# Optimization experiments

Measured on AMD Instinct MI355X. Metric: run time of the kernel, lower is better.

Reference implementation:

```python
import jax, jax.numpy as jnp
import numpy as np

B = 4096
T = 50          # relaxation steps
EPS = 0.5       # epsilon_ep
SCALE = 1.0     # output_scale
CH = [32, 64, 64, 256]


def _conv(x, w, b, stride):
    # NCHW conv, k=3, pad=1 (matches nn.Conv2d(k=3, stride, padding=1))
    y = jax.lax.conv_general_dilated(
        x, w, (stride, stride), [(1, 1), (1, 1)],
        dimension_numbers=("NCHW", "OIHW", "NCHW"))
    return y + b[None, :, None, None]


def _energy(x, s1, s2, s3, s4, vb, w1, b1, w2, b2, w3, b3, w4, b4):
    # E = 0.5*sum||s^n||^2 (incl. x) - Phi_coupling, per sample -> (B,)
    # activation = identity, spectral_scale = 1.0
    n = x.shape[0]
    sq = lambda t: 0.5 * jnp.sum(t.reshape(n, -1) ** 2, axis=1)
    quad = sq(x) + sq(s1) + sq(s2) + sq(s3) + sq(s4)
    dot = lambda a, c: jnp.sum((a * c).reshape(n, -1), axis=1)
    phi = dot(vb, x)                              # visible bias term
    phi = phi + dot(s1, _conv(x, w1, b1, 2))      # s1 . w1(s0)
    phi = phi + dot(s2, _conv(s1, w2, b2, 2))     # s2 . w2(s1)
    phi = phi + dot(s3, _conv(s2, w3, b3, 1))     # s3 . w3(s2)
    phi = phi + jnp.sum(s4 * (s3.reshape(n, -1) @ w4.T + b4), axis=1)
    return quad - phi


def setup_inputs() -> dict:
    key = jax.random.key(0)
    ks = jax.random.split(key, 6)
    x = jax.random.normal(ks[0], (B, 1, 28, 28), jnp.float32)
    # scaled-down Xavier-ish init so the identity-activation relaxation contracts
    def w(k, shape, fan_in):
        return jax.random.normal(k, shape, jnp.float32) * np.float32(0.5 / np.sqrt(fan_in))
    w1 = w(ks[1], (CH[0], 1, 3, 3), 1 * 9)
    w2 = w(ks[2], (CH[1], CH[0], 3, 3), CH[0] * 9)
    w3 = w(ks[3], (CH[2], CH[1], 3, 3), CH[1] * 9)
    w4 = w(ks[4], (CH[3], CH[2] * 7 * 7), CH[2] * 49)
    vb = jax.random.normal(ks[5], (1, 1, 28, 28), jnp.float32) * 0.01
    return dict(x=x, vb=vb,
                w1=w1, b1=jnp.zeros((CH[0],), jnp.float32),
                w2=w2, b2=jnp.zeros((CH[1],), jnp.float32),
                w3=w3, b3=jnp.zeros((CH[2],), jnp.float32),
                w4=w4, b4=jnp.zeros((CH[3],), jnp.float32))


def reference(x, vb, w1, b1, w2, b2, w3, b3, w4, b4):
    n = x.shape[0]
    s0 = (jnp.zeros((n, CH[0], 14, 14), jnp.float32),
          jnp.zeros((n, CH[1], 7, 7), jnp.float32),
          jnp.zeros((n, CH[2], 7, 7), jnp.float32),
          jnp.zeros((n, CH[3]), jnp.float32))

    def e_sum(s):
        return jnp.sum(_energy(x, s[0], s[1], s[2], s[3],
                               vb, w1, b1, w2, b2, w3, b3, w4, b4))

    def step(s, _):
        g = jax.grad(e_sum)(s)
        return tuple(si - EPS * gi for si, gi in zip(s, g)), None

    s_star, _ = jax.lax.scan(step, s0, None, length=T)
    out = _energy(x, s_star[0], s_star[1], s_star[2], s_star[3],
                  vb, w1, b1, w2, b2, w3, b3, w4, b4) * SCALE
    return out  # (B,)
```

## Files before the change

kernel.cpp:

```cpp
#include <hip/hip_runtime.h>
#include <cstddef>


typedef unsigned short ushort_t;
typedef __attribute__((ext_vector_type(8))) short bf8_t;
typedef __attribute__((ext_vector_type(4))) float f4_t;

#define MFMA16 __builtin_amdgcn_mfma_f32_16x16x32_bf16

#define NBn 832
#define NITER 50
#define GPL 5218304u

#define SELG 13125632u
#define R1G 399360
#define R2G 6043648
#define R3G 9877504
#define R4G 12912640

#define W2F_OFF 0u
#define W2B_OFF 36864u
#define W3F_OFF 73728u
#define W3B_OFF 147456u
#define W4P_OFF 221184u
#define W4Q_OFF 1826816u
#define W2PL 18432u
#define W3PL 36864u
#define W4PL 802816u
#define ZOFF 3432448u
#define WPTOT2 3435008u

__device__ __forceinline__ void bsplit(float v, ushort_t& h, ushort_t& lo) {
  union { float f; unsigned u; } a; a.f = v;
  unsigned uh = (a.u + 0x7fffu + ((a.u >> 16) & 1u)) & 0xffff0000u;
  h = (ushort_t)(uh >> 16);
  union { unsigned u; float f; } b; b.u = uh;
  float r = v - b.f;
  union { float f; unsigned u; } c; c.f = r;
  lo = (ushort_t)((c.u + 0x7fffu + ((c.u >> 16) & 1u)) >> 16);
}

__device__ __forceinline__ ushort_t bround(float v) {
  union { float f; unsigned u; } a; a.f = v;
  return (ushort_t)((a.u + 0x7fffu + ((a.u >> 16) & 1u)) >> 16);
}

__device__ __forceinline__ float b2f(ushort_t h) {
  union { unsigned u; float f; } a; a.u = ((unsigned)h) << 16;
  return a.f;
}

__device__ __forceinline__ float bjoin(ushort_t h, ushort_t l) {
  return b2f(h) + b2f(l);
}

__device__ __forceinline__ int xswz(int lin, int nwg) {
  int xcd = lin & 7, o = lin >> 3;
  int q = nwg >> 3, r = nwg & 7;
  return (xcd < r) ? (xcd * (q + 1) + o) : (r * (q + 1) + (xcd - r) * q + o);
}

__global__ void k_fill0(float* p, unsigned n) {
  for (unsigned i = blockIdx.x * blockDim.x + threadIdx.x; i < n;
       i += gridDim.x * blockDim.x)
    p[i] = 0.f;
}

__global__ void k_pack2(const float* __restrict__ w2, ushort_t* __restrict__ WP) {
  int idx = blockIdx.x * blockDim.x + threadIdx.x;
  if (idx >= 18432) return;
  int co = idx / 288, rem = idx % 288, ci = rem / 9, t = rem % 9;
  ushort_t h, l; bsplit(w2[idx], h, l);
  unsigned f = W2F_OFF + t * 2048 + co * 32 + ci;
  unsigned b = W2B_OFF + t * 2048 + ci * 64 + co;
  WP[f] = h; WP[f + W2PL] = l;
  WP[b] = h; WP[b + W2PL] = l;
}

__global__ void k_pack3(const float* __restrict__ w3, ushort_t* __restrict__ WP) {
  int idx = blockIdx.x * blockDim.x + threadIdx.x;
  if (idx >= 36864) return;
  int co = idx / 576, rem = idx % 576, ci = rem / 9, t = rem % 9;
  ushort_t h, l; bsplit(w3[idx], h, l);
  unsigned f = W3F_OFF + t * 4096 + co * 64 + ci;
  unsigned b = W3B_OFF + t * 4096 + ci * 64 + co;
  WP[f] = h; WP[f + W3PL] = l;
  WP[b] = h; WP[b + W3PL] = l;
}

__global__ void k_pack4(const float* __restrict__ w4, ushort_t* __restrict__ WP) {
  int idx = blockIdx.x * blockDim.x + threadIdx.x;
  if (idx >= 802816) return;
  int o = idx / 3136, kk = idx % 3136, c = kk / 49, p = kk % 49;
  ushort_t h, l; bsplit(w4[idx], h, l);
  unsigned a = W4P_OFF + p * 16384 + c * 256 + o;
  unsigned b = W4Q_OFF + o * 3136 + p * 64 + c;
  WP[a] = h; WP[a + W4PL] = l;
  WP[b] = h; WP[b + W4PL] = l;
}

__global__ void k_u1b(ushort_t* __restrict__ G, const float* __restrict__ w1,
                      const float* __restrict__ b1) {
  unsigned idx = blockIdx.x * blockDim.x + threadIdx.x;
  if (idx >= GPL) return;
  int q = idx / 26624, rem = idx % 26624, n = rem / 32, c = rem % 32;
  int oy = q / 14, ox = q % 14;
  float v = 0.f;
  if (n < 784) {
    int py = n / 28, px = n % 28;
    int ky = py - (2 * oy - 1), kx = px - (2 * ox - 1);
    if (ky >= 0 && ky < 3 && kx >= 0 && kx < 3) v = w1[c * 9 + ky * 3 + kx];
  } else if (n == 784) {
    v = b1[c];
  }
  ushort_t h, l; bsplit(v, h, l);
  G[idx] = h; G[idx + GPL] = l;
}

__global__ void k_p1(ushort_t* __restrict__ D, const ushort_t* __restrict__ S,
                     const ushort_t* __restrict__ G) {
  unsigned g8 = (blockIdx.x * blockDim.x + threadIdx.x) * 8;
  if (g8 >= GPL) return;
  size_t off = (size_t)R1G + g8;
  bf8_t oh = *(const bf8_t*)&S[off];
  bf8_t gh = *(const bf8_t*)&G[g8], gl = *(const bf8_t*)&G[g8 + GPL];
  bf8_t rh, rl;
#pragma unroll
  for (int e = 0; e < 8; ++e) {
    float v = 0.5f * b2f((ushort_t)oh[e]) -
              bjoin((ushort_t)gh[e], (ushort_t)gl[e]);
    ushort_t h, l; bsplit(v, h, l);
    rh[e] = (short)h; rl[e] = (short)l;
  }
  *(bf8_t*)&D[off] = rh;
  *(bf8_t*)&D[off + SELG] = rl;
}

struct Ent { unsigned eh, el; int b; int ars, brs; };

__device__ __forceinline__ Ent entry(int role, int e, int p, int mt, int post) {
  Ent E;
  if (role == 3) {
    E.eh = W4Q_OFF + ((unsigned)mt * 64u) * 3136u + (unsigned)e * 32u;
    E.el = E.eh + W4PL;
    E.b = R3G + (e >> 1) * 53248 + (e & 1) * 32;
    E.ars = 3136; E.brs = 64;
  } else if (role == 2) {
    int y = p / 7, x = p % 7;
    if (e < 18) {
      int t = e >> 1, sub = e & 1, ky = t / 3, kx = t % 3;
      int iy = y - 1 + ky, ix = x - 1 + kx;
      bool v = (iy >= 0 && iy < 7 && ix >= 0 && ix < 7);
      E.eh = v ? (W3F_OFF + t * 4096u + sub * 32u) : ZOFF;
      E.el = v ? (E.eh + W3PL) : ZOFF;
      E.b = R2G + (iy * 7 + ix) * 53248 + sub * 32;
      E.ars = v ? 64 : 32; E.brs = 64;
    } else {
      int s = e - 18;
      E.eh = W4P_OFF + (unsigned)p * 16384u + s * 32u;
      E.el = E.eh + W4PL;
      E.b = R4G + s * 32;
      E.ars = 256; E.brs = 256;
    }
  } else if (role == 1) {
    int y = p / 7, x = p % 7;
    if (e < 9) {
      int ky = e / 3, kx = e % 3;
      int iy = 2 * y - 1 + ky, ix = 2 * x - 1 + kx;
      bool v = (iy >= 0 && iy < 14 && ix >= 0 && ix < 14);
      E.eh = v ? (W2F_OFF + e * 2048u) : ZOFF;
      E.el = v ? (E.eh + W2PL) : ZOFF;
      E.b = R1G + (iy * 14 + ix) * 26624;
      E.ars = 32; E.brs = 32;
    } else if (e < 27 && !post) {
      int u = e - 9, t = u >> 1, sub = u & 1, ky = t / 3, kx = t % 3;
      int ty = y + 1 - ky, tx = x + 1 - kx;
      bool v = (ty >= 0 && ty < 7 && tx >= 0 && tx < 7);
      E.eh = v ? (W3B_OFF + t * 4096u + sub * 32u) : ZOFF;
      E.el = v ? (E.eh + W3PL) : ZOFF;
      E.b = R3G + (ty * 7 + tx) * 53248 + sub * 32;
      E.ars = v ? 64 : 32; E.brs = 64;
    } else {
      E.eh = ZOFF; E.el = ZOFF; E.b = R4G; E.ars = 32; E.brs = 256;
    }
  } else {
    int y = p / 14, x = p % 14;
    int tj = e >> 1, sub = e & 1, jy = tj >> 1, jx = tj & 1;
    int ky = (y & 1) ? 2 * jy : 1;
    int kx = (x & 1) ? 2 * jx : 1;
    bool py_ = (y & 1) || (jy == 0);
    bool px_ = (x & 1) || (jx == 0);
    int oy = (y + 1 - ky) >> 1, ox = (x + 1 - kx) >> 1;
    bool v = py_ && px_ && oy >= 0 && oy < 7 && ox >= 0 && ox < 7;
    int t = ky * 3 + kx;
    E.eh = v ? (W2B_OFF + t * 2048u + sub * 32u) : ZOFF;
    E.el = v ? (E.eh + W2PL) : ZOFF;
    E.b = R2G + (oy * 7 + ox) * 53248 + sub * 32;
    E.ars = v ? 64 : 32; E.brs = 64;
  }
  return E;
}

__device__ __forceinline__ Ent entryg(int role, int e, int p, int mt, int post,
                                      int elim) {
  if (e >= elim) {
    Ent E; E.eh = ZOFF; E.el = ZOFF; E.b = R4G; E.ars = 32; E.brs = 256;
    return E;
  }
  return entry(role, e, p, mt, post);
}

template <int APL, int MI>
__device__ __forceinline__ void loadA(bf8_t (&A0)[MI][APL], bf8_t (&A1)[MI][APL],
                                      int role, int e0, int p, int mt, int post,
                                      int elim, int mhalf, int lm, int koff,
                                      const ushort_t* __restrict__ WP) {
  Ent E0 = entryg(role, e0, p, mt, post, elim);
  Ent E1 = entryg(role, e0 + 1, p, mt, post, elim);
#pragma unroll
  for (int mi = 0; mi < MI; ++mi) {
    int mo0 = (mhalf + mi * 16 + lm) * E0.ars + koff;
    int mo1 = (mhalf + mi * 16 + lm) * E1.ars + koff;
    A0[mi][0] = *(const bf8_t*)(WP + E0.eh + mo0);
    A1[mi][0] = *(const bf8_t*)(WP + E1.eh + mo1);
    if (APL == 2) {
      A0[mi][APL - 1] = *(const bf8_t*)(WP + E0.el + mo0);
      A1[mi][APL - 1] = *(const bf8_t*)(WP + E1.el + mo1);
    }
  }
}

__device__ __forceinline__ void loadB(bf8_t& s0, bf8_t& s1, int role, int e0,
                                      int p, int mt, int post, int elim, int n0,
                                      int sn, int sc,
                                      const ushort_t* __restrict__ S) {
  Ent E0 = entryg(role, e0, p, mt, post, elim);
  Ent E1 = entryg(role, e0 + 1, p, mt, post, elim);
  s0 = *(const bf8_t*)(S + E0.b + (n0 + sn) * E0.brs + sc);
  s1 = *(const bf8_t*)(S + E1.b + (n0 + sn) * E1.brs + sc);
}

template <int APL, int MI, int NJ>
__device__ __forceinline__ void mfmaset(const bf8_t (&A0)[MI][APL],
                                        const bf8_t (&A1)[MI][APL],
                                        const ushort_t* __restrict__ Bb, int nhalf,
                                        int lm, int koff, f4_t (&acc)[MI][NJ]) {
#pragma unroll
  for (int nj = 0; nj < NJ; ++nj) {
    int lo = (nhalf + nj * 16 + lm) * 40 + koff;
    bf8_t b0 = *(const bf8_t*)&Bb[lo];
    bf8_t b1 = *(const bf8_t*)&Bb[2560 + lo];
#pragma unroll
    for (int mi = 0; mi < MI; ++mi)
#pragma unroll
      for (int pl = 0; pl < APL; ++pl) {
        acc[mi][nj] = MFMA16(A0[mi][pl], b0, acc[mi][nj], 0, 0, 0);
        acc[mi][nj] = MFMA16(A1[mi][pl], b1, acc[mi][nj], 0, 0, 0);
      }
  }
}

template <int APL, int MI, int NJ>
__device__ __forceinline__ void mloop(int role, int post, int p, int mt, int n0,
                                      int NC2, int mhalf, int nhalf,
                                      const ushort_t* __restrict__ S,
                                      const ushort_t* __restrict__ WP,
                                      ushort_t* __restrict__ SB,
                                      f4_t (&acc)[MI][NJ]) {
  const int tid = threadIdx.x, l = tid & 63;
  const int lm = l & 15, koff = (l >> 4) * 8;
  const int sn = tid >> 2, sc = (tid & 3) * 8;
  const int elim = 2 * NC2;
  bf8_t bs0[4], bs1[4];
#pragma unroll
  for (int q = 0; q < 4; ++q)
    loadB(bs0[q], bs1[q], role, 2 * q, p, mt, post, elim, n0, sn, sc, S);
  bf8_t aE0[MI][APL], aE1[MI][APL], aO0[MI][APL], aO1[MI][APL];
  loadA<APL, MI>(aE0, aE1, role, 0, p, mt, post, elim, mhalf, lm, koff, WP);
  loadA<APL, MI>(aO0, aO1, role, 2, p, mt, post, elim, mhalf, lm, koff, WP);
  {
    int wb = sn * 40 + sc;
    *(bf8_t*)&SB[wb] = bs0[0];
    *(bf8_t*)&SB[wb + 2560] = bs1[0];
  }
  __syncthreads();
  const int ntrip = (NC2 + 3) >> 2;
  for (int t4 = 0; t4 < ntrip; ++t4) {
    int j4 = t4 * 4;
#pragma unroll
    for (int pp = 0; pp < 4; ++pp) {
      int jj = j4 + pp;
      loadB(bs0[pp], bs1[pp], role, 2 * (jj + 4), p, mt, post, elim, n0, sn, sc, S);
      const ushort_t* Bb = SB + (pp & 1) * 5120;
      if ((pp & 1) == 0) {
        mfmaset<APL, MI, NJ>(aE0, aE1, Bb, nhalf, lm, koff, acc);
        loadA<APL, MI>(aE0, aE1, role, 2 * (jj + 2), p, mt, post, elim, mhalf, lm,
                       koff, WP);
      } else {
        mfmaset<APL, MI, NJ>(aO0, aO1, Bb, nhalf, lm, koff, acc);
        loadA<APL, MI>(aO0, aO1, role, 2 * (jj + 2), p, mt, post, elim, mhalf, lm,
                       koff, WP);
      }
      {
        int wb = sn * 40 + sc;
        ushort_t* Wb = SB + ((pp + 1) & 1) * 5120;
        *(bf8_t*)&Wb[wb] = bs0[(pp + 1) & 3];
        *(bf8_t*)&Wb[wb + 2560] = bs1[(pp + 1) & 3];
      }
      __syncthreads();
    }
  }
}

template <int POST>
__global__ __launch_bounds__(256) void k_mega(
    const ushort_t* __restrict__ S, ushort_t* __restrict__ D,
    const ushort_t* __restrict__ G, const ushort_t* __restrict__ WP,
    const float* __restrict__ b2, const float* __restrict__ b3,
    const float* __restrict__ b4) {
  __shared__ __align__(16) ushort_t SB[10240];
  float* Lt = (float*)SB;
  const int tid = threadIdx.x, l = tid & 63, w = tid >> 6;
  const int lm = l & 15, lk = l >> 4;
  int b = blockIdx.x;
  int role, rb, ntile, pq;
  if (b < 52) { role = 3; rb = xswz(b, 52); ntile = rb >> 2; pq = rb & 3; }
  else if (b < 689) { role = 2; rb = xswz(b - 52, 637); ntile = rb / 49; pq = rb % 49; }
  else if (b < 1326) { role = 1; rb = xswz(b - 689, 637); ntile = rb / 49; pq = rb % 49; }
  else { role = 0; rb = xswz(b - 1326, 2548); ntile = rb / 196; pq = rb % 196; }

  int n0 = ntile * 64;

  if (role == 0) {
    f4_t acc[2][1] = {};
    mloop<1, 2, 1>(0, POST, pq, 0, n0, 4, 0, w * 16, S, WP, SB, acc);
    __syncthreads();
#pragma unroll
    for (int mi = 0; mi < 2; ++mi)
#pragma unroll
      for (int r = 0; r < 4; ++r)
        Lt[(w * 16 + lm) * 33 + mi * 16 + lk * 4 + r] = acc[mi][0][r];
    __syncthreads();
    int nl = tid >> 2, cq = (tid & 3) * 8;
    int n = n0 + nl;
    size_t off = (size_t)R1G + (size_t)pq * 26624 + (size_t)n * 32 + cq;
    size_t goff = (size_t)pq * 26624 + (size_t)n * 32 + cq;
    bf8_t oh = *(const bf8_t*)&S[off];
    bf8_t gh = *(const bf8_t*)&G[goff], gl = *(const bf8_t*)&G[goff + GPL];
    const float* lp = Lt + nl * 33 + cq;
    bf8_t rh;
#pragma unroll
    for (int e = 0; e < 8; ++e) {
      float old = b2f((ushort_t)oh[e]);
      float u = bjoin((ushort_t)gh[e], (ushort_t)gl[e]);
      rh[e] = (short)bround(0.5f * old + 0.5f * (lp[e] + u));
    }
    *(bf8_t*)&D[off] = rh;
  } else {
    f4_t acc[2][2] = {};
    int NC2 = (role == 3) ? 49 : (role == 2) ? (POST ? 9 : 13) : (POST ? 5 : 14);
    mloop<POST + 1, 2, 2>(role, POST, pq, pq, n0, NC2, (w & 1) * 32, (w >> 1) * 32,
                          S, WP, SB, acc);
    __syncthreads();
#pragma unroll
    for (int mi = 0; mi < 2; ++mi)
#pragma unroll
      for (int nj = 0; nj < 2; ++nj)
#pragma unroll
        for (int r = 0; r < 4; ++r)
          Lt[((w >> 1) * 32 + nj * 16 + lm) * 65 + (w & 1) * 32 + mi * 16 + lk * 4 + r] =
              acc[mi][nj][r];
    __syncthreads();
    int nl = tid >> 2, cq = (tid & 3) * 16;
    int n = n0 + nl;
    size_t off;
    const float* bias;
    int bq = cq;
    if (role == 1) { off = (size_t)R2G + (size_t)pq * 53248 + (size_t)n * 64 + cq; bias = b2; }
    else if (role == 2) { off = (size_t)R3G + (size_t)pq * 53248 + (size_t)n * 64 + cq; bias = b3; }
    else { off = (size_t)R4G + (size_t)n * 256 + pq * 64 + cq; bias = b4; bq = pq * 64 + cq; }
    const float* lp = Lt + nl * 65 + cq;
#pragma unroll
    for (int half = 0; half < 2; ++half) {
      size_t o8 = off + half * 8;
      bf8_t oh = *(const bf8_t*)&S[o8];
      bf8_t rh, rl;
#pragma unroll
      for (int e = 0; e < 8; ++e) {
        float v = lp[half * 8 + e];
        if (n == 784) v += bias[bq + half * 8 + e];
        float old = b2f((ushort_t)oh[e]);
        if (POST) {
          float nv = 0.5f * old - v;
          ushort_t h, l2; bsplit(nv, h, l2);
          rh[e] = (short)h; rl[e] = (short)l2;
        } else {
          rh[e] = (short)bround(0.5f * old + 0.5f * v);
        }
      }
      *(bf8_t*)&D[o8] = rh;
      if (POST) *(bf8_t*)&D[o8 + SELG] = rl;
    }
  }
}

__device__ __forceinline__ void hstep(int s, size_t& base, int& C, int& c0) {
  if (s < 196) { base = R1G + (size_t)s * 26624; C = 32; c0 = 0; }
  else if (s < 294) { int u = s - 196; base = R2G + (size_t)(u >> 1) * 53248; C = 64; c0 = (u & 1) * 32; }
  else if (s < 392) { int u = s - 294; base = R3G + (size_t)(u >> 1) * 53248; C = 64; c0 = (u & 1) * 32; }
  else { base = R4G; C = 256; c0 = (s - 392) * 32; }
}

struct HF { bf8_t ah[4]; bf8_t al[4]; bf8_t b[4]; };

__device__ __forceinline__ void hload(HF& F, int s, int m0, int n0, int lm, int koff,
                                      const ushort_t* __restrict__ P,
                                      const ushort_t* __restrict__ S) {
  size_t base; int C, c0;
  hstep(s, base, C, c0);
#pragma unroll
  for (int mi = 0; mi < 4; ++mi) {
    const ushort_t* Am = P + base + (size_t)(m0 + mi * 16 + lm) * C + c0 + koff;
    F.ah[mi] = *(const bf8_t*)Am;
    F.al[mi] = *(const bf8_t*)(Am + SELG);
  }
#pragma unroll
  for (int nj = 0; nj < 4; ++nj)
    F.b[nj] = *(const bf8_t*)(S + base + (size_t)(n0 + nj * 16 + lm) * C + c0 + koff);
}

__device__ __forceinline__ void hmfma(HF& F, f4_t (&acc)[4][4]) {
#pragma unroll
  for (int mi = 0; mi < 4; ++mi)
#pragma unroll
    for (int nj = 0; nj < 4; ++nj) {
      acc[mi][nj] = MFMA16(F.ah[mi], F.b[nj], acc[mi][nj], 0, 0, 0);
      acc[mi][nj] = MFMA16(F.al[mi], F.b[nj], acc[mi][nj], 0, 0, 0);
    }
}

__global__ __launch_bounds__(256) void k_hgemm(float* __restrict__ HpT,
                                               const ushort_t* __restrict__ P,
                                               const ushort_t* __restrict__ S) {
  int tid = threadIdx.x, l = tid & 63, w = tid >> 6;
  int lm = l & 15, lk = l >> 4, koff = lk * 8;
  int m0 = blockIdx.y * 128 + (w & 1) * 64;
  int n0 = blockIdx.x * 128 + (w >> 1) * 64;
  int z = blockIdx.z;
  int s0 = (400 * z) / 9, s1e = (400 * (z + 1)) / 9;
  int ns = s1e - s0;
  f4_t acc[4][4] = {};
  HF F0, F1;
  hload(F0, s0, m0, n0, lm, koff, P, S);
  hload(F1, (ns > 1) ? s0 + 1 : s0, m0, n0, lm, koff, P, S);
  int t = 0;
  for (; t + 2 <= ns; t += 2) {
    hmfma(F0, acc);
    hload(F0, (s0 + t + 2 < s1e) ? s0 + t + 2 : s1e - 1, m0, n0, lm, koff, P, S);
    hmfma(F1, acc);
    hload(F1, (s0 + t + 3 < s1e) ? s0 + t + 3 : s1e - 1, m0, n0, lm, koff, P, S);
  }
  if (t < ns) hmfma(F0, acc);
#pragma unroll
  for (int mi = 0; mi < 4; ++mi)
#pragma unroll
    for (int nj = 0; nj < 4; ++nj)
#pragma unroll
      for (int r = 0; r < 4; ++r) {
        int m = m0 + mi * 16 + lk * 4 + r;
        int n = n0 + nj * 16 + lm;
        if (m < NBn && n < NBn)
          HpT[((size_t)z * NBn + n) * NBn + m] = acc[mi][nj][r];
      }
}

__global__ void k_combT(ushort_t* __restrict__ HtH, ushort_t* __restrict__ HtL,
                        const float* __restrict__ HpT) {
  int idx = blockIdx.x * blockDim.x + threadIdx.x;
  if (idx >= NBn * NBn) return;
  float s = 0.f;
#pragma unroll
  for (int z = 0; z < 9; ++z) s += HpT[(size_t)z * NBn * NBn + idx];
  ushort_t h, l; bsplit(s, h, l);
  HtH[idx] = h; HtL[idx] = l;
}

__global__ void k_xsplit(ushort_t* __restrict__ XH, ushort_t* __restrict__ XL,
                         const float* __restrict__ x, int Bn) {
  int idx = blockIdx.x * blockDim.x + threadIdx.x;
  if (idx >= Bn * NBn) return;
  int i = idx / NBn, j = idx % NBn;
  float v = (j < 784) ? x[(size_t)i * 784 + j] : (j == 784 ? 1.f : 0.f);
  ushort_t h, l; bsplit(v, h, l);
  XH[idx] = h; XL[idx] = l;
}

__global__ __launch_bounds__(256) void k_ygemm(float* __restrict__ Y,
    const ushort_t* __restrict__ XH, const ushort_t* __restrict__ XL,
    const ushort_t* __restrict__ HtH, const ushort_t* __restrict__ HtL, int Bn) {
  int tid = threadIdx.x, l = tid & 63, w = tid >> 6;
  int lm = l & 15, lk = l >> 4, koff = lk * 8;
  int m0 = blockIdx.y * 64 + (w & 1) * 32;
  int n0 = blockIdx.x * 64 + (w >> 1) * 32;
  f4_t acc[2][2] = {};
  for (int k0 = 0; k0 < NBn; k0 += 32) {
    bf8_t bh[2], bl[2];
#pragma unroll
    for (int nj = 0; nj < 2; ++nj) {
      size_t bo = (size_t)(n0 + nj * 16 + lm) * NBn + k0 + koff;
      bh[nj] = *(const bf8_t*)(HtH + bo);
      bl[nj] = *(const bf8_t*)(HtL + bo);
    }
#pragma unroll
    for (int mi = 0; mi < 2; ++mi) {
      int mrow = m0 + mi * 16 + lm;
      if (mrow >= Bn) mrow = Bn - 1;
      size_t ao = (size_t)mrow * NBn + k0 + koff;
      bf8_t ah = *(const bf8_t*)(XH + ao);
      bf8_t al = *(const bf8_t*)(XL + ao);
#pragma unroll
      for (int nj = 0; nj < 2; ++nj) {
        acc[mi][nj] = MFMA16(ah, bh[nj], acc[mi][nj], 0, 0, 0);
        acc[mi][nj] = MFMA16(ah, bl[nj], acc[mi][nj], 0, 0, 0);
        acc[mi][nj] = MFMA16(al, bh[nj], acc[mi][nj], 0, 0, 0);
      }
    }
  }
#pragma unroll
  for (int mi = 0; mi < 2; ++mi)
#pragma unroll
    for (int nj = 0; nj < 2; ++nj)
#pragma unroll
      for (int r = 0; r < 4; ++r) {
        int m = m0 + mi * 16 + lk * 4 + r;
        int n = n0 + nj * 16 + lm;
        if (m < Bn) Y[(size_t)m * NBn + n] = acc[mi][nj][r];
      }
}

__global__ void k_out(float* __restrict__ out, const float* __restrict__ x,
                      const float* __restrict__ vb, const float* __restrict__ Y, int Bn) {
  int wave = threadIdx.x >> 6, lane = threadIdx.x & 63;
  int i = blockIdx.x * 4 + wave;
  if (i >= Bn) return;
  const float* xi = x + (size_t)i * 784;
  const float* yi = Y + (size_t)i * NBn;
  float s = 0.f;
  for (int j = lane; j < 784; j += 64) {
    float xv = xi[j];
    s += xv * (0.5f * xv - vb[j] + yi[j]);
  }
  for (int off = 32; off; off >>= 1) s += __shfl_down(s, off);
  if (lane == 0) out[i] = s + yi[784];
}

extern "C" void kernel_launch(void* const* d_in, const int* in_sizes, int n_in, void* d_out,
                              int out_size, void* d_ws, size_t ws_size, hipStream_t stream) {
  const float* x  = (const float*)d_in[0];
  const float* vb = (const float*)d_in[1];
  const float* w1 = (const float*)d_in[2];
  const float* b1 = (const float*)d_in[3];
  const float* w2 = (const float*)d_in[4];
  const float* b2 = (const float*)d_in[5];
  const float* w3 = (const float*)d_in[6];
  const float* b3 = (const float*)d_in[7];
  const float* w4 = (const float*)d_in[8];
  const float* b4 = (const float*)d_in[9];
  int Bn = in_sizes[0] / 784;
  float* out = (float*)d_out;

  ushort_t* S0 = (ushort_t*)d_ws;
  ushort_t* S1 = S0 + (size_t)SELG;
  ushort_t* Pb = S1 + (size_t)SELG;
  ushort_t* G  = Pb + (size_t)2 * SELG;
  ushort_t* WP = G + (size_t)2 * GPL;
  ushort_t* HtH = WP + WPTOT2;
  ushort_t* HtL = HtH + (size_t)NBn * NBn;
  float* HpT = (float*)S1;
  ushort_t* XH = Pb;
  ushort_t* XL = XH + (size_t)Bn * NBn;
  float* Y = (float*)G;

  const int TB = 256;
  k_fill0<<<2048, TB, 0, stream>>>((float*)S0, SELG / 2);
  k_fill0<<<2048, TB, 0, stream>>>((float*)S1, SELG / 2);
  k_fill0<<<2, TB, 0, stream>>>((float*)(WP + ZOFF), 1280);
  k_pack2<<<72, TB, 0, stream>>>(w2, WP);
  k_pack3<<<144, TB, 0, stream>>>(w3, WP);
  k_pack4<<<3136, TB, 0, stream>>>(w4, WP);
  k_u1b<<<20384, TB, 0, stream>>>(G, w1, b1);

  ushort_t* cur = S0;
  ushort_t* nxt = S1;
  for (int it = 0; it < NITER; ++it) {
    k_mega<0><<<3874, TB, 0, stream>>>(cur, nxt, G, WP, b2, b3, b4);
    ushort_t* t = cur; cur = nxt; nxt = t;
  }

  k_p1<<<2548, TB, 0, stream>>>(Pb, cur, G);
  k_mega<1><<<1326, TB, 0, stream>>>(cur, Pb, G, WP, b2, b3, b4);

  k_hgemm<<<dim3(7, 7, 9), TB, 0, stream>>>(HpT, Pb, cur);
  k_combT<<<(NBn * NBn + TB - 1) / TB, TB, 0, stream>>>(HtH, HtL, HpT);

  k_xsplit<<<(Bn * NBn + TB - 1) / TB, TB, 0, stream>>>(XH, XL, x, Bn);
  k_ygemm<<<dim3(13, (Bn + 63) / 64), TB, 0, stream>>>(Y, XH, XL, HtH, HtL, Bn);
  k_out<<<(Bn + 3) / 4, TB, 0, stream>>>(out, x, vb, Y, Bn);
}
```

Measured before the change: 3.609 ms.

## Process two K-steps per LDS stage to halve barriers in GEMM main loop

Restructures the software pipeline of the shared GEMM loop so each LDS buffer holds two K-slices and each barrier covers two MFMA sets instead of one. The LDS tile grows to double capacity and the global prefetch is reorganized into two ping-pong register sets. This aims to halve __syncthreads overhead per K, at the cost of more LDS per block, which may reduce occupancy. Odd slice counts may be handled less cleanly.

```diff
diff --git a/kernel.cpp b/kernel.cpp
--- a/kernel.cpp
+++ b/kernel.cpp
@@ -271,42 +271,61 @@
   const int lm = l & 15, koff = (l >> 4) * 8;
   const int sn = tid >> 2, sc = (tid & 3) * 8;
   const int elim = 2 * NC2;
-  bf8_t bs0[4], bs1[4];
-#pragma unroll
-  for (int q = 0; q < 4; ++q)
-    loadB(bs0[q], bs1[q], role, 2 * q, p, mt, post, elim, n0, sn, sc, S);
+  const int wb = sn * 40 + sc;
+  bf8_t pA0[2], pA1[2], pB0[2], pB1[2];
+#pragma unroll
+  for (int q = 0; q < 2; ++q)
+    loadB(pA0[q], pA1[q], role, 2 * q, p, mt, post, elim, n0, sn, sc, S);
+#pragma unroll
+  for (int q = 0; q < 2; ++q)
+    loadB(pB0[q], pB1[q], role, 4 + 2 * q, p, mt, post, elim, n0, sn, sc, S);
   bf8_t aE0[MI][APL], aE1[MI][APL], aO0[MI][APL], aO1[MI][APL];
   loadA<APL, MI>(aE0, aE1, role, 0, p, mt, post, elim, mhalf, lm, koff, WP);
   loadA<APL, MI>(aO0, aO1, role, 2, p, mt, post, elim, mhalf, lm, koff, WP);
   {
-    int wb = sn * 40 + sc;
-    *(bf8_t*)&SB[wb] = bs0[0];
-    *(bf8_t*)&SB[wb + 2560] = bs1[0];
-  }
+    *(bf8_t*)&SB[wb] = pA0[0];         *(bf8_t*)&SB[wb + 2560] = pA1[0];
+    *(bf8_t*)&SB[wb + 5120] = pA0[1];  *(bf8_t*)&SB[wb + 7680] = pA1[1];
+  }
+#pragma unroll
+  for (int q = 0; q < 2; ++q)
+    loadB(pA0[q], pA1[q], role, 8 + 2 * q, p, mt, post, elim, n0, sn, sc, S);
   __syncthreads();
-  const int ntrip = (NC2 + 3) >> 2;
-  for (int t4 = 0; t4 < ntrip; ++t4) {
-    int j4 = t4 * 4;
-#pragma unroll
-    for (int pp = 0; pp < 4; ++pp) {
-      int jj = j4 + pp;
-      loadB(bs0[pp], bs1[pp], role, 2 * (jj + 4), p, mt, post, elim, n0, sn, sc, S);
-      const ushort_t* Bb = SB + (pp & 1) * 5120;
-      if ((pp & 1) == 0) {
-        mfmaset<APL, MI, NJ>(aE0, aE1, Bb, nhalf, lm, koff, acc);
-        loadA<APL, MI>(aE0, aE1, role, 2 * (jj + 2), p, mt, post, elim, mhalf, lm,
-                       koff, WP);
-      } else {
-        mfmaset<APL, MI, NJ>(aO0, aO1, Bb, nhalf, lm, koff, acc);
-        loadA<APL, MI>(aO0, aO1, role, 2 * (jj + 2), p, mt, post, elim, mhalf, lm,
-                       koff, WP);
-      }
-      {
-        int wb = sn * 40 + sc;
-        ushort_t* Wb = SB + ((pp + 1) & 1) * 5120;
-        *(bf8_t*)&Wb[wb] = bs0[(pp + 1) & 3];
-        *(bf8_t*)&Wb[wb + 2560] = bs1[(pp + 1) & 3];
-      }
+  const int NS = (NC2 + 1) >> 1;
+  const int ntrip = (NS + 1) >> 1;
+  for (int tt = 0; tt < ntrip; ++tt) {
+    const int t0 = tt * 2;
+    {
+      const ushort_t* Bb = SB;
+      mfmaset<APL, MI, NJ>(aE0, aE1, Bb, nhalf, lm, koff, acc);
+      loadA<APL, MI>(aE0, aE1, role, 4 * (t0 + 1), p, mt, post, elim, mhalf, lm,
+                     koff, WP);
+      mfmaset<APL, MI, NJ>(aO0, aO1, Bb + 5120, nhalf, lm, koff, acc);
+      loadA<APL, MI>(aO0, aO1, role, 4 * (t0 + 1) + 2, p, mt, post, elim, mhalf,
+                     lm, koff, WP);
+      ushort_t* Wb = SB + 10240;
+      *(bf8_t*)&Wb[wb] = pB0[0];         *(bf8_t*)&Wb[wb + 2560] = pB1[0];
+      *(bf8_t*)&Wb[wb + 5120] = pB0[1];  *(bf8_t*)&Wb[wb + 7680] = pB1[1];
+#pragma unroll
+      for (int q = 0; q < 2; ++q)
+        loadB(pB0[q], pB1[q], role, 4 * (t0 + 3) + 2 * q, p, mt, post, elim, n0,
+              sn, sc, S);
+      __syncthreads();
+    }
+    {
+      const ushort_t* Bb = SB + 10240;
+      mfmaset<APL, MI, NJ>(aE0, aE1, Bb, nhalf, lm, koff, acc);
+      loadA<APL, MI>(aE0, aE1, role, 4 * (t0 + 2), p, mt, post, elim, mhalf, lm,
+                     koff, WP);
+      mfmaset<APL, MI, NJ>(aO0, aO1, Bb + 5120, nhalf, lm, koff, acc);
+      loadA<APL, MI>(aO0, aO1, role, 4 * (t0 + 2) + 2, p, mt, post, elim, mhalf,
+                     lm, koff, WP);
+      ushort_t* Wb = SB;
+      *(bf8_t*)&Wb[wb] = pA0[0];         *(bf8_t*)&Wb[wb + 2560] = pA1[0];
+      *(bf8_t*)&Wb[wb + 5120] = pA0[1];  *(bf8_t*)&Wb[wb + 7680] = pA1[1];
+#pragma unroll
+      for (int q = 0; q < 2; ++q)
+        loadB(pA0[q], pA1[q], role, 4 * (t0 + 4) + 2 * q, p, mt, post, elim, n0,
+              sn, sc, S);
       __syncthreads();
     }
   }
@@ -318,7 +337,7 @@
     const ushort_t* __restrict__ G, const ushort_t* __restrict__ WP,
     const float* __restrict__ b2, const float* __restrict__ b3,
     const float* __restrict__ b4) {
-  __shared__ __align__(16) ushort_t SB[10240];
+  __shared__ __align__(16) ushort_t SB[20480];
   float* Lt = (float*)SB;
   const int tid = threadIdx.x, l = tid & 63, w = tid >> 6;
   const int lm = l & 15, lk = l >> 4;
```

Result: no change. 3.641 ms (+0.9%).

## Compute layer-1 transposed-conv update per 2x2 output quad sharing s2 tiles

Applied to the files above, without the earlier changes.

The role-0 blocks, which update s1 via the transposed w2 convolution, now each cover a 2x2 group of 14x14 output positions for one 7x7 s2 location instead of one output position. The four neighbouring s2 tiles are loaded into shared memory once and reused across the four parity positions, cutting redundant B loads and the block count from 3874 to 1963. Shared memory per block doubles to 20480 elements, which may lower occupancy, and each block does more serial work.

```diff
diff --git a/kernel.cpp b/kernel.cpp
--- a/kernel.cpp
+++ b/kernel.cpp
@@ -162,7 +162,7 @@
       E.b = R4G + s * 32;
       E.ars = 256; E.brs = 256;
     }
-  } else if (role == 1) {
+  } else {
     int y = p / 7, x = p % 7;
     if (e < 9) {
       int ky = e / 3, kx = e % 3;
@@ -183,20 +183,6 @@
     } else {
       E.eh = ZOFF; E.el = ZOFF; E.b = R4G; E.ars = 32; E.brs = 256;
     }
-  } else {
-    int y = p / 14, x = p % 14;
-    int tj = e >> 1, sub = e & 1, jy = tj >> 1, jx = tj & 1;
-    int ky = (y & 1) ? 2 * jy : 1;
-    int kx = (x & 1) ? 2 * jx : 1;
-    bool py_ = (y & 1) || (jy == 0);
-    bool px_ = (x & 1) || (jx == 0);
-    int oy = (y + 1 - ky) >> 1, ox = (x + 1 - kx) >> 1;
-    bool v = py_ && px_ && oy >= 0 && oy < 7 && ox >= 0 && ox < 7;
-    int t = ky * 3 + kx;
-    E.eh = v ? (W2B_OFF + t * 2048u + sub * 32u) : ZOFF;
-    E.el = v ? (E.eh + W2PL) : ZOFF;
-    E.b = R2G + (oy * 7 + ox) * 53248 + sub * 32;
-    E.ars = v ? 64 : 32; E.brs = 64;
   }
   return E;
 }
@@ -318,7 +304,7 @@
     const ushort_t* __restrict__ G, const ushort_t* __restrict__ WP,
     const float* __restrict__ b2, const float* __restrict__ b3,
     const float* __restrict__ b4) {
-  __shared__ __align__(16) ushort_t SB[10240];
+  __shared__ __align__(16) ushort_t SB[20480];
   float* Lt = (float*)SB;
   const int tid = threadIdx.x, l = tid & 63, w = tid >> 6;
   const int lm = l & 15, lk = l >> 4;
@@ -327,35 +313,80 @@
   if (b < 52) { role = 3; rb = xswz(b, 52); ntile = rb >> 2; pq = rb & 3; }
   else if (b < 689) { role = 2; rb = xswz(b - 52, 637); ntile = rb / 49; pq = rb % 49; }
   else if (b < 1326) { role = 1; rb = xswz(b - 689, 637); ntile = rb / 49; pq = rb % 49; }
-  else { role = 0; rb = xswz(b - 1326, 2548); ntile = rb / 196; pq = rb % 196; }
+  else { role = 0; rb = xswz(b - 1326, 637); ntile = rb / 49; pq = rb % 49; }
 
   int n0 = ntile * 64;
 
   if (role == 0) {
-    f4_t acc[2][1] = {};
-    mloop<1, 2, 1>(0, POST, pq, 0, n0, 4, 0, w * 16, S, WP, SB, acc);
+    const int Y = pq / 7, X = pq % 7;
+    const int sn = tid >> 2, sc = (tid & 3) * 8;
+    const int koff = lk * 8;
+    bf8_t breg[8];
+#pragma unroll
+    for (int e = 0; e < 8; ++e) {
+      int t2 = e >> 1, dy = t2 >> 1, dx = t2 & 1, sub = e & 1;
+      bool tv = (Y + dy < 7) && (X + dx < 7);
+      int bbase = tv ? (R2G + ((Y + dy) * 7 + (X + dx)) * 53248 + sub * 32) : R4G;
+      breg[e] = *(const bf8_t*)(S + bbase + (n0 + sn) * 64 + sc);
+    }
+    {
+      int wb = sn * 40 + sc;
+#pragma unroll
+      for (int e = 0; e < 8; ++e) *(bf8_t*)&SB[e * 2560 + wb] = breg[e];
+    }
     __syncthreads();
-#pragma unroll
-    for (int mi = 0; mi < 2; ++mi)
-#pragma unroll
-      for (int r = 0; r < 4; ++r)
-        Lt[(w * 16 + lm) * 33 + mi * 16 + lk * 4 + r] = acc[mi][0][r];
-    __syncthreads();
-    int nl = tid >> 2, cq = (tid & 3) * 8;
-    int n = n0 + nl;
-    size_t off = (size_t)R1G + (size_t)pq * 26624 + (size_t)n * 32 + cq;
-    size_t goff = (size_t)pq * 26624 + (size_t)n * 32 + cq;
-    bf8_t oh = *(const bf8_t*)&S[off];
-    bf8_t gh = *(const bf8_t*)&G[goff], gl = *(const bf8_t*)&G[goff + GPL];
-    const float* lp = Lt + nl * 33 + cq;
-    bf8_t rh;
+    f4_t acc[4][2] = {};
+    const int nloc = w * 16 + lm;
 #pragma unroll
     for (int e = 0; e < 8; ++e) {
-      float old = b2f((ushort_t)oh[e]);
-      float u = bjoin((ushort_t)gh[e], (ushort_t)gl[e]);
-      rh[e] = (short)bround(0.5f * old + 0.5f * (lp[e] + u));
-    }
-    *(bf8_t*)&D[off] = rh;
+      int t2 = e >> 1, dy = t2 >> 1, dx = t2 & 1, sub = e & 1;
+      bool tv = (Y + dy < 7) && (X + dx < 7);
+      bf8_t bfr = *(const bf8_t*)&SB[e * 2560 + nloc * 40 + koff];
+#pragma unroll
+      for (int py = 0; py < 2; ++py) {
+#pragma unroll
+        for (int px = 0; px < 2; ++px) {
+          const int ky = py + 1 - 2 * dy, kx = px + 1 - 2 * dx;
+          if (ky >= 0 && kx >= 0) {
+            unsigned abase = tv ? (W2B_OFF + (unsigned)(ky * 3 + kx) * 2048u +
+                                   (unsigned)sub * 32u)
+                                : ZOFF;
+            const int pos = py * 2 + px;
+#pragma unroll
+            for (int mi = 0; mi < 2; ++mi) {
+              bf8_t afr = *(const bf8_t*)(WP + abase + (mi * 16 + lm) * 64 + koff);
+              acc[pos][mi] = MFMA16(afr, bfr, acc[pos][mi], 0, 0, 0);
+            }
+          }
+        }
+      }
+    }
+#pragma unroll
+    for (int pos = 0; pos < 4; ++pos) {
+      __syncthreads();
+#pragma unroll
+      for (int mi = 0; mi < 2; ++mi)
+#pragma unroll
+        for (int r = 0; r < 4; ++r)
+          Lt[(w * 16 + lm) * 33 + mi * 16 + lk * 4 + r] = acc[pos][mi][r];
+      __syncthreads();
+      int q = (2 * Y + (pos >> 1)) * 14 + 2 * X + (pos & 1);
+      int nl = tid >> 2, cq = (tid & 3) * 8;
+      int n = n0 + nl;
+      size_t off = (size_t)R1G + (size_t)q * 26624 + (size_t)n * 32 + cq;
+      size_t goff = (size_t)q * 26624 + (size_t)n * 32 + cq;
+      bf8_t oh = *(const bf8_t*)&S[off];
+      bf8_t gh = *(const bf8_t*)&G[goff], gl = *(const bf8_t*)&G[goff + GPL];
+      const float* lp = Lt + nl * 33 + cq;
+      bf8_t rh;
+#pragma unroll
+      for (int e = 0; e < 8; ++e) {
+        float old = b2f((ushort_t)oh[e]);
+        float u = bjoin((ushort_t)gh[e], (ushort_t)gl[e]);
+        rh[e] = (short)bround(0.5f * old + 0.5f * (lp[e] + u));
+      }
+      *(bf8_t*)&D[off] = rh;
+    }
   } else {
     f4_t acc[2][2] = {};
     int NC2 = (role == 3) ? 49 : (role == 2) ? (POST ? 9 : 13) : (POST ? 5 : 14);
@@ -593,7 +624,7 @@
   ushort_t* cur = S0;
   ushort_t* nxt = S1;
   for (int it = 0; it < NITER; ++it) {
-    k_mega<0><<<3874, TB, 0, stream>>>(cur, nxt, G, WP, b2, b3, b4);
+    k_mega<0><<<1963, TB, 0, stream>>>(cur, nxt, G, WP, b2, b3, b4);
     ushort_t* t = cur; cur = nxt; nxt = t;
   }
 
```

Result: faster. 3.531 ms, median of 2 (-2.2%).
